# Kernel tuning notes

Measured on AMD Instinct MI355X. Metric: run time of the kernel, lower is better.

Reference implementation:

```python
import jax, jax.numpy as jnp
import numpy as np
from jax import lax

B, T = 64, 2048
D_ENC, D_RNN, D_ATT = 512, 1024, 128
NF, K = 32, 31


def setup_inputs() -> dict:
    key = jax.random.key(0)
    ks = jax.random.split(key, 9)
    return {
        "attention_hidden_state": jax.random.normal(ks[0], (B, D_RNN), jnp.float32),
        "memory": jax.random.normal(ks[1], (B, T, D_ENC), jnp.float32),
        "processed_memory": jax.random.normal(ks[2], (B, T, D_ATT), jnp.float32),
        "attention_weights_cat": jax.random.uniform(ks[3], (B, 2, T), jnp.float32),
        "mask": jnp.zeros((B, T), dtype=bool),
        "query_w": jax.random.normal(ks[4], (D_ATT, D_RNN), jnp.float32) * 0.02,
        "value_w": jax.random.normal(ks[5], (1, D_ATT), jnp.float32) * 0.05,
        "loc_conv_w": jax.random.normal(ks[6], (NF, 2, K), jnp.float32) * 0.1,
        "loc_dense_w": jax.random.normal(ks[7], (D_ATT, NF), jnp.float32) * 0.1,
    }


def reference(attention_hidden_state, memory, processed_memory,
              attention_weights_cat, mask, query_w, value_w,
              loc_conv_w, loc_dense_w):
    k = loc_conv_w.shape[-1]
    pad = (k - 1) // 2
    # processed query: [B, 1, D_ATT]
    pq = (attention_hidden_state @ query_w.T)[:, None, :]
    # location features: Conv1d(2->NF, 'same' pad, no bias) then dense NF->D_ATT
    loc = lax.conv_general_dilated(
        attention_weights_cat, loc_conv_w,
        window_strides=(1,), padding=[(pad, pad)],
        dimension_numbers=("NCH", "OIH", "NCH"))  # [B, NF, T]
    loc = jnp.einsum("bft,af->bta", loc, loc_dense_w)  # [B, T, D_ATT]
    # additive energies
    energies = jnp.tanh(pq + processed_memory + loc)  # [B, T, D_ATT]
    alignment = jnp.einsum("bta,a->bt", energies, value_w[0])  # [B, T]
    alignment = jnp.where(mask, -jnp.inf, alignment)
    attention_weights = jax.nn.softmax(alignment, axis=1)  # [B, T]
    attention_context = jnp.einsum("bt,btd->bd", attention_weights, memory)
    return attention_context, attention_weights
```

## Files before the change

kernel.cpp:

```cpp
#include <hip/hip_runtime.h>
#include <hip/hip_bf16.h>

#define BB 64
#define TT 2048
#define D_ENC 512
#define D_RNN 1024
#define D_ATT 128
#define NF 32
#define KW 31

__device__ __forceinline__ float fast_tanh(float x) {
    float e = __expf(2.0f * x);
    return 1.0f - __fdividef(2.0f, e + 1.0f);
}

__global__ __launch_bounds__(256) void pq_kernel(
    const float* __restrict__ hid, const float* __restrict__ qw,
    float* __restrict__ pq)
{
    int b = blockIdx.x;
    int wave = threadIdx.x >> 6, lane = threadIdx.x & 63;
    int a = blockIdx.y * 4 + wave;
    const float* hrow = hid + (size_t)b * D_RNN;
    const float* qrow = qw + (size_t)a * D_RNN;
    float acc = 0.f;
#pragma unroll
    for (int j = 0; j < 4; ++j) {
        int k = (j * 64 + lane) * 4;
        float4 h = *(const float4*)(hrow + k);
        float4 q = *(const float4*)(qrow + k);
        acc += h.x * q.x + h.y * q.y + h.z * q.z + h.w * q.w;
    }
#pragma unroll
    for (int off = 32; off; off >>= 1) acc += __shfl_xor(acc, off, 64);
    if (lane == 0) pq[b * D_ATT + a] = acc;
}

__global__ __launch_bounds__(256) void align_kernel(
    const float* __restrict__ pm,
    const float* __restrict__ awcat,
    const unsigned char* __restrict__ mask,
    const float* __restrict__ convw,
    const float* __restrict__ ldw,
    const float* __restrict__ vw,
    const float* __restrict__ pq,
    float* __restrict__ align_out)
{
    __shared__ float s_aw[2 * 160];
    __shared__ float s_loc[128 * NF];

    int b = blockIdx.x;
    int t0 = blockIdx.y * 128;
    int tid = threadIdx.x;

    for (int i = tid; i < 320; i += 256) {
        int c = i / 160, j = i % 160;
        int tg = t0 - 15 + j;
        float v = 0.f;
        if (tg >= 0 && tg < TT) v = awcat[((size_t)b * 2 + c) * TT + tg];
        s_aw[c * 160 + j] = v;
    }
    __syncthreads();

    {
        int f = tid & 31, g = tid >> 5;
        float w[2 * KW];
#pragma unroll
        for (int j = 0; j < 2 * KW; ++j) w[j] = convw[f * 2 * KW + j];
#pragma unroll
        for (int p = 0; p < 4; ++p) {
            int tb = g * 16 + p * 4;
            float a0 = 0.f, a1 = 0.f, a2 = 0.f, a3 = 0.f;
#pragma unroll
            for (int c = 0; c < 2; ++c) {
                float x[34];
#pragma unroll
                for (int j = 0; j < 34; ++j) x[j] = s_aw[c * 160 + tb + j];
#pragma unroll
                for (int k = 0; k < KW; ++k) {
                    float wk = w[c * KW + k];
                    a0 += x[k] * wk; a1 += x[k + 1] * wk;
                    a2 += x[k + 2] * wk; a3 += x[k + 3] * wk;
                }
            }
            s_loc[(tb + 0) * NF + f] = a0;
            s_loc[(tb + 1) * NF + f] = a1;
            s_loc[(tb + 2) * NF + f] = a2;
            s_loc[(tb + 3) * NF + f] = a3;
        }
    }
    __syncthreads();

    int wave = tid >> 6, lane = tid & 63;
    float pq0 = pq[b * 128 + lane], pq1 = pq[b * 128 + 64 + lane];
    float vw0 = vw[lane], vw1 = vw[64 + lane];
    float4 lA[8], lB[8];
#pragma unroll
    for (int f4 = 0; f4 < 8; ++f4) {
        lA[f4] = *(const float4*)(ldw + lane * NF + f4 * 4);
        lB[f4] = *(const float4*)(ldw + (64 + lane) * NF + f4 * 4);
    }
    const float* pmb = pm + ((size_t)b * TT + t0) * 128;
    for (int i = 0; i < 32; ++i) {
        int t = wave * 32 + i;
        float pm0 = pmb[(size_t)t * 128 + lane];
        float pm1 = pmb[(size_t)t * 128 + 64 + lane];
        float dA = 0.f, dB = 0.f;
#pragma unroll
        for (int f4 = 0; f4 < 8; ++f4) {
            float4 lv = *(const float4*)&s_loc[t * NF + f4 * 4];
            dA += lv.x * lA[f4].x + lv.y * lA[f4].y + lv.z * lA[f4].z + lv.w * lA[f4].w;
            dB += lv.x * lB[f4].x + lv.y * lB[f4].y + lv.z * lB[f4].z + lv.w * lB[f4].w;
        }
        float eA = fast_tanh(pq0 + pm0 + dA);
        float eB = fast_tanh(pq1 + pm1 + dB);
        float al = vw0 * eA + vw1 * eB;
#pragma unroll
        for (int off = 32; off; off >>= 1) al += __shfl_xor(al, off, 64);
        if (lane == 0) {
            int tt = t0 + t;
            bool m = mask[(size_t)b * TT + tt] != 0;
            align_out[(size_t)b * TT + tt] = m ? -__builtin_inff() : al;
        }
    }
}

__global__ __launch_bounds__(256) void softmax_kernel(float* __restrict__ wts)
{
    int b = blockIdx.x;
    int tid = threadIdx.x;
    float* row = wts + (size_t)b * TT;
    float v[8];
    float mx = -__builtin_inff();
#pragma unroll
    for (int i = 0; i < 8; ++i) { v[i] = row[tid + i * 256]; mx = fmaxf(mx, v[i]); }
    __shared__ float s_red[8];
    int wave = tid >> 6, lane = tid & 63;
#pragma unroll
    for (int off = 32; off; off >>= 1) mx = fmaxf(mx, __shfl_xor(mx, off, 64));
    if (lane == 0) s_red[wave] = mx;
    __syncthreads();
    mx = fmaxf(fmaxf(s_red[0], s_red[1]), fmaxf(s_red[2], s_red[3]));
    float sum = 0.f;
#pragma unroll
    for (int i = 0; i < 8; ++i) { v[i] = __expf(v[i] - mx); sum += v[i]; }
#pragma unroll
    for (int off = 32; off; off >>= 1) sum += __shfl_xor(sum, off, 64);
    if (lane == 0) s_red[4 + wave] = sum;
    __syncthreads();
    sum = s_red[4] + s_red[5] + s_red[6] + s_red[7];
    float inv = __fdividef(1.0f, sum);
#pragma unroll
    for (int i = 0; i < 8; ++i) row[tid + i * 256] = v[i] * inv;
}

__global__ __launch_bounds__(256) void ctx_kernel(
    const float* __restrict__ mem, const float* __restrict__ wts,
    float* __restrict__ out)
{
    int b = blockIdx.x, c = blockIdx.y;
    int tid = threadIdx.x;
    int d4 = tid & 127;
    int th = tid >> 7;
    int t0 = c * 128;
    const float* wrow = wts + (size_t)b * TT + t0;
    const float4* mrow = (const float4*)(mem + ((size_t)b * TT + t0) * D_ENC);
    float4 acc = {0.f, 0.f, 0.f, 0.f};
    for (int i = th; i < 128; i += 2) {
        float w = wrow[i];
        float4 m = mrow[(size_t)i * 128 + d4];
        acc.x += w * m.x; acc.y += w * m.y; acc.z += w * m.z; acc.w += w * m.w;
    }
    __shared__ float4 s_p[128];
    if (th == 1) s_p[d4] = acc;
    __syncthreads();
    if (th == 0) {
        float4 o = s_p[d4];
        float* dst = out + (size_t)b * D_ENC + d4 * 4;
        atomicAdd(dst + 0, acc.x + o.x);
        atomicAdd(dst + 1, acc.y + o.y);
        atomicAdd(dst + 2, acc.z + o.z);
        atomicAdd(dst + 3, acc.w + o.w);
    }
}

extern "C" void kernel_launch(void* const* d_in, const int* in_sizes, int n_in,
                              void* d_out, int out_size, void* d_ws, size_t ws_size,
                              hipStream_t stream)
{
    const float* hid  = (const float*)d_in[0];
    const float* mem  = (const float*)d_in[1];
    const float* pm   = (const float*)d_in[2];
    const float* aw   = (const float*)d_in[3];
    const unsigned char* mask = (const unsigned char*)d_in[4];
    const float* qw   = (const float*)d_in[5];
    const float* vw   = (const float*)d_in[6];
    const float* cw   = (const float*)d_in[7];
    const float* ldw  = (const float*)d_in[8];

    float* out = (float*)d_out;
    float* ctx = out;
    float* wts = out + BB * D_ENC;
    float* pq  = (float*)d_ws;

    hipMemsetAsync(ctx, 0, (size_t)BB * D_ENC * sizeof(float), stream);
    pq_kernel<<<dim3(BB, 32), 256, 0, stream>>>(hid, qw, pq);
    align_kernel<<<dim3(BB, TT / 128), 256, 0, stream>>>(pm, aw, mask, cw, ldw, vw, pq, wts);
    softmax_kernel<<<BB, 256, 0, stream>>>(wts);
    ctx_kernel<<<dim3(BB, 16), 256, 0, stream>>>(mem, wts, ctx);
}
```

Before: 492.3 us.

## Fuse alignment, unnormalized softmax and context reduction into one kernel

Merges the alignment, softmax and context kernels into one fused kernel. It computes exp of the alignment directly, without subtracting the max, and accumulates the context and per-batch exponent sums with atomics. A small finalize kernel then rescales the weights and context by the inverse sum. This removes the extra kernel launches and the global round trip of the alignment weights. The cost is relying on bounded energies so exp does not overflow, plus extra atomics.

```diff
diff --git a/kernel.cpp b/kernel.cpp
--- a/kernel.cpp
+++ b/kernel.cpp
@@ -9,11 +9,6 @@
 #define NF 32
 #define KW 31
 
-__device__ __forceinline__ float fast_tanh(float x) {
-    float e = __expf(2.0f * x);
-    return 1.0f - __fdividef(2.0f, e + 1.0f);
-}
-
 __global__ __launch_bounds__(256) void pq_kernel(
     const float* __restrict__ hid, const float* __restrict__ qw,
     float* __restrict__ pq)
@@ -36,7 +31,7 @@
     if (lane == 0) pq[b * D_ATT + a] = acc;
 }
 
-__global__ __launch_bounds__(256) void align_kernel(
+__global__ __launch_bounds__(256) void fused_kernel(
     const float* __restrict__ pm,
     const float* __restrict__ awcat,
     const unsigned char* __restrict__ mask,
@@ -44,10 +39,15 @@
     const float* __restrict__ ldw,
     const float* __restrict__ vw,
     const float* __restrict__ pq,
-    float* __restrict__ align_out)
+    const float* __restrict__ mem,
+    float* __restrict__ wts,
+    float* __restrict__ ctx,
+    float* __restrict__ sums)
 {
     __shared__ float s_aw[2 * 160];
     __shared__ float s_loc[128 * NF];
+    __shared__ float s_e[128];
+    __shared__ float4 s_p[128];
 
     int b = blockIdx.x;
     int t0 = blockIdx.y * 128;
@@ -91,97 +91,87 @@
     }
     __syncthreads();
 
-    int wave = tid >> 6, lane = tid & 63;
-    float pq0 = pq[b * 128 + lane], pq1 = pq[b * 128 + 64 + lane];
-    float vw0 = vw[lane], vw1 = vw[64 + lane];
-    float4 lA[8], lB[8];
-#pragma unroll
-    for (int f4 = 0; f4 < 8; ++f4) {
-        lA[f4] = *(const float4*)(ldw + lane * NF + f4 * 4);
-        lB[f4] = *(const float4*)(ldw + (64 + lane) * NF + f4 * 4);
-    }
-    const float* pmb = pm + ((size_t)b * TT + t0) * 128;
-    for (int i = 0; i < 32; ++i) {
-        int t = wave * 32 + i;
-        float pm0 = pmb[(size_t)t * 128 + lane];
-        float pm1 = pmb[(size_t)t * 128 + 64 + lane];
-        float dA = 0.f, dB = 0.f;
+    {
+        int wave = tid >> 6, lane = tid & 63;
+        float pq0 = pq[b * 128 + lane], pq1 = pq[b * 128 + 64 + lane];
+        float vw0 = vw[lane], vw1 = vw[64 + lane];
+        float4 lA[8], lB[8];
 #pragma unroll
         for (int f4 = 0; f4 < 8; ++f4) {
-            float4 lv = *(const float4*)&s_loc[t * NF + f4 * 4];
-            dA += lv.x * lA[f4].x + lv.y * lA[f4].y + lv.z * lA[f4].z + lv.w * lA[f4].w;
-            dB += lv.x * lB[f4].x + lv.y * lB[f4].y + lv.z * lB[f4].z + lv.w * lB[f4].w;
-        }
-        float eA = fast_tanh(pq0 + pm0 + dA);
-        float eB = fast_tanh(pq1 + pm1 + dB);
-        float al = vw0 * eA + vw1 * eB;
-#pragma unroll
-        for (int off = 32; off; off >>= 1) al += __shfl_xor(al, off, 64);
-        if (lane == 0) {
-            int tt = t0 + t;
-            bool m = mask[(size_t)b * TT + tt] != 0;
-            align_out[(size_t)b * TT + tt] = m ? -__builtin_inff() : al;
-        }
-    }
-}
-
-__global__ __launch_bounds__(256) void softmax_kernel(float* __restrict__ wts)
-{
-    int b = blockIdx.x;
-    int tid = threadIdx.x;
-    float* row = wts + (size_t)b * TT;
-    float v[8];
-    float mx = -__builtin_inff();
-#pragma unroll
-    for (int i = 0; i < 8; ++i) { v[i] = row[tid + i * 256]; mx = fmaxf(mx, v[i]); }
-    __shared__ float s_red[8];
-    int wave = tid >> 6, lane = tid & 63;
-#pragma unroll
-    for (int off = 32; off; off >>= 1) mx = fmaxf(mx, __shfl_xor(mx, off, 64));
-    if (lane == 0) s_red[wave] = mx;
+            lA[f4] = *(const float4*)(ldw + lane * NF + f4 * 4);
+            lB[f4] = *(const float4*)(ldw + (64 + lane) * NF + f4 * 4);
+        }
+        const float* pmb = pm + ((size_t)b * TT + t0) * 128;
+        for (int i = 0; i < 32; ++i) {
+            int t = wave * 32 + i;
+            float pm0 = pmb[(size_t)t * 128 + lane];
+            float pm1 = pmb[(size_t)t * 128 + 64 + lane];
+            float dA = 0.f, dB = 0.f;
+#pragma unroll
+            for (int f4 = 0; f4 < 8; ++f4) {
+                float4 lv = *(const float4*)&s_loc[t * NF + f4 * 4];
+                dA += lv.x * lA[f4].x + lv.y * lA[f4].y + lv.z * lA[f4].z + lv.w * lA[f4].w;
+                dB += lv.x * lB[f4].x + lv.y * lB[f4].y + lv.z * lB[f4].z + lv.w * lB[f4].w;
+            }
+            float xA = pq0 + pm0 + dA, xB = pq1 + pm1 + dB;
+            float eA = 1.0f - __fdividef(2.0f, __expf(2.0f * xA) + 1.0f);
+            float eB = 1.0f - __fdividef(2.0f, __expf(2.0f * xB) + 1.0f);
+            float al = vw0 * eA + vw1 * eB;
+#pragma unroll
+            for (int off = 32; off; off >>= 1) al += __shfl_xor(al, off, 64);
+            if (lane == 0) {
+                int tt = t0 + t;
+                bool m = mask[(size_t)b * TT + tt] != 0;
+                float e = m ? 0.f : __expf(al);
+                s_e[t] = e;
+                wts[(size_t)b * TT + tt] = e;
+            }
+        }
+    }
     __syncthreads();
-    mx = fmaxf(fmaxf(s_red[0], s_red[1]), fmaxf(s_red[2], s_red[3]));
-    float sum = 0.f;
-#pragma unroll
-    for (int i = 0; i < 8; ++i) { v[i] = __expf(v[i] - mx); sum += v[i]; }
-#pragma unroll
-    for (int off = 32; off; off >>= 1) sum += __shfl_xor(sum, off, 64);
-    if (lane == 0) s_red[4 + wave] = sum;
-    __syncthreads();
-    sum = s_red[4] + s_red[5] + s_red[6] + s_red[7];
-    float inv = __fdividef(1.0f, sum);
-#pragma unroll
-    for (int i = 0; i < 8; ++i) row[tid + i * 256] = v[i] * inv;
-}
-
-__global__ __launch_bounds__(256) void ctx_kernel(
-    const float* __restrict__ mem, const float* __restrict__ wts,
-    float* __restrict__ out)
-{
-    int b = blockIdx.x, c = blockIdx.y;
-    int tid = threadIdx.x;
-    int d4 = tid & 127;
-    int th = tid >> 7;
-    int t0 = c * 128;
-    const float* wrow = wts + (size_t)b * TT + t0;
-    const float4* mrow = (const float4*)(mem + ((size_t)b * TT + t0) * D_ENC);
-    float4 acc = {0.f, 0.f, 0.f, 0.f};
-    for (int i = th; i < 128; i += 2) {
-        float w = wrow[i];
-        float4 m = mrow[(size_t)i * 128 + d4];
-        acc.x += w * m.x; acc.y += w * m.y; acc.z += w * m.z; acc.w += w * m.w;
-    }
-    __shared__ float4 s_p[128];
-    if (th == 1) s_p[d4] = acc;
-    __syncthreads();
-    if (th == 0) {
-        float4 o = s_p[d4];
-        float* dst = out + (size_t)b * D_ENC + d4 * 4;
-        atomicAdd(dst + 0, acc.x + o.x);
-        atomicAdd(dst + 1, acc.y + o.y);
-        atomicAdd(dst + 2, acc.z + o.z);
-        atomicAdd(dst + 3, acc.w + o.w);
-    }
+
+    if (tid < 64) {
+        float s = s_e[tid] + s_e[tid + 64];
+#pragma unroll
+        for (int off = 32; off; off >>= 1) s += __shfl_xor(s, off, 64);
+        if (tid == 0) atomicAdd(&sums[b], s);
+    }
+
+    {
+        int d4 = tid & 127;
+        int th = tid >> 7;
+        const float4* mrow = (const float4*)(mem + ((size_t)b * TT + t0) * D_ENC);
+        float4 acc = {0.f, 0.f, 0.f, 0.f};
+        for (int i = th; i < 128; i += 2) {
+            float w = s_e[i];
+            float4 m = mrow[(size_t)i * 128 + d4];
+            acc.x += w * m.x; acc.y += w * m.y; acc.z += w * m.z; acc.w += w * m.w;
+        }
+        if (th == 1) s_p[d4] = acc;
+        __syncthreads();
+        if (th == 0) {
+            float4 o = s_p[d4];
+            float* dst = ctx + (size_t)b * D_ENC + d4 * 4;
+            atomicAdd(dst + 0, acc.x + o.x);
+            atomicAdd(dst + 1, acc.y + o.y);
+            atomicAdd(dst + 2, acc.z + o.z);
+            atomicAdd(dst + 3, acc.w + o.w);
+        }
+    }
+}
+
+__global__ __launch_bounds__(256) void finalize_kernel(
+    float* __restrict__ wts, float* __restrict__ ctx,
+    const float* __restrict__ sums)
+{
+    int b = blockIdx.x, tid = threadIdx.x;
+    float inv = __fdividef(1.0f, sums[b]);
+    float* wrow = wts + (size_t)b * TT;
+#pragma unroll
+    for (int i = 0; i < 8; ++i) wrow[tid + i * 256] *= inv;
+    float* crow = ctx + (size_t)b * D_ENC;
+    crow[tid] *= inv;
+    crow[tid + 256] *= inv;
 }
 
 extern "C" void kernel_launch(void* const* d_in, const int* in_sizes, int n_in,
@@ -202,10 +192,12 @@
     float* ctx = out;
     float* wts = out + BB * D_ENC;
     float* pq  = (float*)d_ws;
+    float* sums = pq + BB * D_ATT;
 
     hipMemsetAsync(ctx, 0, (size_t)BB * D_ENC * sizeof(float), stream);
+    hipMemsetAsync(sums, 0, (size_t)BB * sizeof(float), stream);
     pq_kernel<<<dim3(BB, 32), 256, 0, stream>>>(hid, qw, pq);
-    align_kernel<<<dim3(BB, TT / 128), 256, 0, stream>>>(pm, aw, mask, cw, ldw, vw, pq, wts);
-    softmax_kernel<<<BB, 256, 0, stream>>>(wts);
-    ctx_kernel<<<dim3(BB, 16), 256, 0, stream>>>(mem, wts, ctx);
-}
+    fused_kernel<<<dim3(BB, TT / 128), 256, 0, stream>>>(
+        pm, aw, mask, cw, ldw, vw, pq, mem, wts, ctx, sums);
+    finalize_kernel<<<BB, 256, 0, stream>>>(wts, ctx, sums);
+}
```

New measurement: 503.8 us. +2.3%, slower.
